# Kernel tuning notes

Measured on AMD Instinct MI355X. Metric: run time of the kernel, lower is better.

Reference implementation:

```python
import jax, jax.numpy as jnp
import numpy as np
import math

B, S, D, H = 2, 2048, 1024, 16
HD = D // H  # head_dims = 64


def setup_inputs() -> dict:
    key = jax.random.key(0)
    ks = jax.random.split(key, 8)
    sc = 1.0 / math.sqrt(D)
    return {
        "queries": jax.random.normal(ks[0], (B, S, D), jnp.float32),
        "keys":    jax.random.normal(ks[1], (B, S, D), jnp.float32),
        "values":  jax.random.normal(ks[2], (B, S, D), jnp.float32),
        # causal mask: 1 where attending allowed, 0 where blocked (masked_fill on ==0)
        "mask": jnp.tril(jnp.ones((S, S), jnp.int32)),
        "Wq": jax.random.normal(ks[3], (D, D), jnp.float32) * sc,
        "bq": jnp.zeros((D,), jnp.float32),
        "Wk": jax.random.normal(ks[4], (D, D), jnp.float32) * sc,
        "bk": jnp.zeros((D,), jnp.float32),
        "Wv": jax.random.normal(ks[5], (D, D), jnp.float32) * sc,
        "bv": jnp.zeros((D,), jnp.float32),
        "Wo": jax.random.normal(ks[6], (D, D), jnp.float32) * sc,
        "bo": jnp.zeros((D,), jnp.float32),
    }


def _split_heads(x):
    # (B, S, D) -> (B, H, S, HD)
    return x.reshape(B, S, H, HD).transpose(0, 2, 1, 3)


def reference(queries, keys, values, mask, Wq, bq, Wk, bk, Wv, bv, Wo, bo):
    q = queries @ Wq + bq
    k = keys @ Wk + bk
    # NOTE: faithful to source quirk — V is projected from the ALREADY-PROJECTED keys
    # (original: keys = self.W_keys(keys); values = self.W_values(keys))
    v = k @ Wv + bv
    q, k, v = _split_heads(q), _split_heads(k), _split_heads(v)
    # naive full NxN attention, as in the source
    scores = jnp.einsum("bhqd,bhkd->bhqk", q, k) / math.sqrt(HD)
    scores = jnp.where(mask == 0, jnp.float32(-1e9), scores)
    probs = jax.nn.softmax(scores, axis=-1)
    attn = jnp.einsum("bhqk,bhkd->bhqd", probs, v)
    attn = attn.transpose(0, 2, 1, 3).reshape(B, S, D)
    return attn @ Wo + bo
```

## Files before the change

kernel.cpp:

```cpp
#include <hip/hip_runtime.h>

typedef unsigned short u16;
typedef unsigned int u32;
typedef __bf16 bf16x8 __attribute__((ext_vector_type(8)));
typedef float f32x4 __attribute__((ext_vector_type(4)));
typedef float f32x16 __attribute__((ext_vector_type(16)));
typedef unsigned int u32x4v __attribute__((ext_vector_type(4)));

#define MFMA16(a, b, c) __builtin_amdgcn_mfma_f32_16x16x32_bf16(a, b, c, 0, 0, 0)
#define MFMA32(a, b, c) __builtin_amdgcn_mfma_f32_32x32x16_bf16(a, b, c, 0, 0, 0)

__device__ __forceinline__ void gload16(const void* g, void* l) {
  __builtin_amdgcn_global_load_lds((const __attribute__((address_space(1))) void*)g,
                                   (__attribute__((address_space(3))) void*)l, 16, 0, 0);
}

__device__ __forceinline__ u16 f2bf(float f) {
  u32 u = __builtin_bit_cast(u32, f);
  u += 0x7fffu + ((u >> 16) & 1u);
  return (u16)(u >> 16);
}
__device__ __forceinline__ u32 pack2(float a, float b) {
  u32 r;
  asm("v_cvt_pk_bf16_f32 %0, %1, %2" : "=v"(r) : "v"(a), "v"(b));
  return r;
}

__global__ __launch_bounds__(256) void cvt_kernel(const float* __restrict__ q,
                                                  const float* __restrict__ k,
                                                  u16* __restrict__ qb,
                                                  u16* __restrict__ kb) {
  const float* src = blockIdx.y ? k : q;
  u16* dst = blockIdx.y ? kb : qb;
  size_t i = (size_t)blockIdx.x * 256 + threadIdx.x;
  float4 v = ((const float4*)src)[i];
  uint2 o;
  o.x = pack2(v.x, v.y);
  o.y = pack2(v.z, v.w);
  ((uint2*)dst)[i] = o;
}

__global__ __launch_bounds__(256) void wtrans_kernel(const float* W0, const float* W1,
                                                     const float* W2, const float* W3,
                                                     u16* T0, u16* T1, u16* T2, u16* T3) {
  int z = blockIdx.z;
  const float* W = z == 0 ? W0 : z == 1 ? W1 : z == 2 ? W2 : W3;
  u16* T = z == 0 ? T0 : z == 1 ? T1 : z == 2 ? T2 : T3;
  __shared__ float tile[64][65];
  int tr = blockIdx.y * 64, tc = blockIdx.x * 64;
  int tid = threadIdx.x;
  int c4 = (tid & 15) * 4, r0 = tid >> 4;
#pragma unroll
  for (int i = 0; i < 4; i++) {
    int r = r0 + i * 16;
    float4 v = *(const float4*)(W + (size_t)(tr + r) * 1024 + tc + c4);
    tile[r][c4 + 0] = v.x; tile[r][c4 + 1] = v.y;
    tile[r][c4 + 2] = v.z; tile[r][c4 + 3] = v.w;
  }
  __syncthreads();
#pragma unroll
  for (int i = 0; i < 2; i++) {
    int c = tid + i * 256;
    int n = c >> 3, kg = c & 7;
    uint4 o;
    o.x = pack2(tile[kg * 8 + 0][n], tile[kg * 8 + 1][n]);
    o.y = pack2(tile[kg * 8 + 2][n], tile[kg * 8 + 3][n]);
    o.z = pack2(tile[kg * 8 + 4][n], tile[kg * 8 + 5][n]);
    o.w = pack2(tile[kg * 8 + 6][n], tile[kg * 8 + 7][n]);
    *(uint4*)(T + (size_t)(tc + n) * 1024 + tr + kg * 8) = o;
  }
}

template <int MODE>
__global__ __launch_bounds__(256) void gemm_kernel(
    const u16* A0, const u16* B0, const float* bias0, void* C0, float scale0,
    const u16* A1, const u16* B1, const float* bias1, void* C1, float scale1,
    int M, int N, int K) {
  const u16* A = A0; const u16* Bt = B0; const float* bias = bias0; void* Cout = C0;
  float scale = scale0;
  if (blockIdx.z) { A = A1; Bt = B1; bias = bias1; Cout = C1; scale = scale1; }

  __shared__ __attribute__((aligned(16))) char sAB[49152];
  const int tid = threadIdx.x, lane = tid & 63, w = tid >> 6;
  const int l15 = lane & 15, quad = lane >> 4;
  const int wm = (w >> 1) * 64, wn = (w & 1) * 32;
  const int m0 = blockIdx.y * 128, n0 = blockIdx.x * 64;

  const int lrow = lane >> 3, lcg = (lane & 7) ^ lrow;
  const u16* aP[4]; const u16* bP[2];
#pragma unroll
  for (int i = 0; i < 4; i++)
    aP[i] = A + (size_t)(m0 + w * 32 + i * 8 + lrow) * K + lcg * 8;
#pragma unroll
  for (int i = 0; i < 2; i++)
    bP[i] = Bt + (size_t)(n0 + w * 16 + i * 8 + lrow) * K + lcg * 8;

  int aoff[4], boff[2];
#pragma unroll
  for (int t = 0; t < 4; t++) {
    int ra = wm + t * 16 + l15;
    aoff[t] = ra * 128 + ((quad ^ (ra & 7)) * 16);
  }
#pragma unroll
  for (int t = 0; t < 2; t++) {
    int rb = wn + t * 16 + l15;
    boff[t] = 16384 + rb * 128 + ((quad ^ (rb & 7)) * 16);
  }

#pragma unroll
  for (int i = 0; i < 4; i++) { gload16(aP[i], sAB + w * 4096 + i * 1024); aP[i] += 64; }
#pragma unroll
  for (int i = 0; i < 2; i++) { gload16(bP[i], sAB + 16384 + w * 2048 + i * 1024); bP[i] += 64; }

  f32x4 acc[4][2] = {};
  int cur = 0;
  for (int k = 0; k < K; k += 64) {
    __syncthreads();
    if (k + 64 < K) {
      char* dst = sAB + (cur ^ 1) * 24576;
#pragma unroll
      for (int i = 0; i < 4; i++) { gload16(aP[i], dst + w * 4096 + i * 1024); aP[i] += 64; }
#pragma unroll
      for (int i = 0; i < 2; i++) { gload16(bP[i], dst + 16384 + w * 2048 + i * 1024); bP[i] += 64; }
    }
    const char* buf = sAB + cur * 24576;
#pragma unroll
    for (int kt = 0; kt < 2; kt++) {
      bf16x8 af[4], bfr[2];
#pragma unroll
      for (int t = 0; t < 4; t++) af[t] = *(const bf16x8*)(buf + (aoff[t] ^ (kt * 64)));
#pragma unroll
      for (int t = 0; t < 2; t++) bfr[t] = *(const bf16x8*)(buf + (boff[t] ^ (kt * 64)));
#pragma unroll
      for (int mt = 0; mt < 4; mt++)
#pragma unroll
        for (int nt = 0; nt < 2; nt++)
          acc[mt][nt] = MFMA16(af[mt], bfr[nt], acc[mt][nt]);
    }
    cur ^= 1;
  }

#pragma unroll
  for (int nt = 0; nt < 2; nt++) {
    int col = n0 + wn + nt * 16 + l15;
    float bv = bias[col];
#pragma unroll
    for (int mt = 0; mt < 4; mt++) {
      int row = m0 + wm + mt * 16 + quad * 4;
      if (MODE == 0) {
        u16* C = (u16*)Cout;
#pragma unroll
        for (int r = 0; r < 4; r++)
          C[(size_t)(row + r) * N + col] = f2bf((acc[mt][nt][r] + bv) * scale);
      } else if (MODE == 1) {
        u16* C = (u16*)Cout;
        int hh = col >> 6, hd = col & 63;
        int bb = row >> 11, s = row & 2047;
        uint2 o;
        o.x = pack2((acc[mt][nt][0] + bv) * scale, (acc[mt][nt][1] + bv) * scale);
        o.y = pack2((acc[mt][nt][2] + bv) * scale, (acc[mt][nt][3] + bv) * scale);
        *(uint2*)(C + ((size_t)((bb * 16 + hh) * 64 + hd) * 2048 + s)) = o;
      } else {
        float* C = (float*)Cout;
#pragma unroll
        for (int r = 0; r < 4; r++)
          C[(size_t)(row + r) * N + col] = (acc[mt][nt][r] + bv) * scale;
      }
    }
  }
}

__global__ __launch_bounds__(256, 2) void attn_kernel(const u16* __restrict__ qw,
                                                      const u16* __restrict__ kw,
                                                      const u16* __restrict__ vw,
                                                      u16* __restrict__ aout) {
  __shared__ __attribute__((aligned(16))) char sKV[4][16384];
  __shared__ float slq[4][64];
  char* sflat = (char*)sKV;
  const int bh = blockIdx.x, p = blockIdx.y;
  const int b = bh >> 4, h = bh & 15;
  const int tid = threadIdx.x, lane = tid & 63, w = tid >> 6;
  const int g = w & 1, kh = w >> 1;
  const int c = lane & 31, hi = lane >> 5;
  const int lrow = lane >> 3, lcg = (lane & 7) ^ lrow;
  const u16* kb0 = kw + (size_t)(b * 2048) * 1024 + h * 64;
  const u16* vb0 = vw + (size_t)bh * 64 * 2048;

  int koffK[4], koffV[2][2];
  {
    int krow = kh * 32 + c;
#pragma unroll
    for (int kt = 0; kt < 4; kt++)
      koffK[kt] = krow * 128 + (((kt * 2 + hi) ^ (krow & 7)) * 16);
#pragma unroll
    for (int m = 0; m < 2; m++) {
      int vrow = m * 32 + c;
#pragma unroll
      for (int kt2 = 0; kt2 < 2; kt2++)
        koffV[m][kt2] = 8192 + vrow * 128 + ((((kh * 2 + kt2) * 2 + hi) ^ (vrow & 7)) * 16);
    }
  }

  auto stage = [&](int j, int slot) {
    char* dst = sKV[slot];
#pragma unroll
    for (int i = 0; i < 2; i++) {
      int rr = w * 16 + i * 8 + lrow;
      gload16(kb0 + (size_t)(j * 64 + rr) * 1024 + lcg * 8, dst + w * 2048 + i * 1024);
      gload16(vb0 + (size_t)rr * 2048 + j * 64 + lcg * 8, dst + 8192 + w * 2048 + i * 1024);
    }
  };

  for (int phase = 0; phase < 2; ++phase) {
    const int t = phase ? (31 - p) : p;
    __syncthreads();

    bf16x8 qf[2][4];
#pragma unroll
    for (int qb2 = 0; qb2 < 2; qb2++) {
      const u16* qbase =
          qw + (size_t)(b * 2048 + t * 64 + qb2 * 32 + c) * 1024 + h * 64 + hi * 8;
#pragma unroll
      for (int kt = 0; kt < 4; kt++) qf[qb2][kt] = *(const bf16x8*)(qbase + kt * 16);
    }
    stage(0, 0);
    if (t >= 1) stage(1, 1);

    f32x16 o00 = {}, o01 = {}, o10 = {}, o11 = {};
    float ls0 = 0.f, ls1 = 0.f;
    const int R = (t + 2) >> 1;
    for (int r = 0; r < R; ++r) {
      __syncthreads();
      if (2 * r + 2 <= t) stage(2 * r + 2, (2 * r + 2) & 3);
      if (2 * r + 3 <= t) stage(2 * r + 3, (2 * r + 3) & 3);
      const int jg = 2 * r + g;
      if (jg <= t) {
        const char* buf = sKV[jg & 3];
        f32x16 S0 = {}, S1 = {};
        __builtin_amdgcn_s_setprio(1);
#pragma unroll
        for (int kt = 0; kt < 4; kt++) {
          bf16x8 kf = *(const bf16x8*)(buf + koffK[kt]);
          S0 = MFMA32(kf, qf[0][kt], S0);
          S1 = MFMA32(kf, qf[1][kt], S1);
        }
        __builtin_amdgcn_s_setprio(0);
        const bool diag = (jg == t);
        u32 pw0[8], pw1[8];
        auto epack = [&](const f32x16& S, int qc, u32* pw, float& ls) {
          float e[16];
#pragma unroll
          for (int rg = 0; rg < 16; rg++) {
            float ev = __builtin_amdgcn_exp2f(S[rg]);
            if (diag) {
              int row = kh * 32 + (rg & 3) + 8 * (rg >> 2) + 4 * hi;
              if (row > qc) ev = 0.f;
            }
            e[rg] = ev;
          }
          float s = 0.f;
#pragma unroll
          for (int rg = 0; rg < 16; rg += 4)
            s += (e[rg] + e[rg + 1]) + (e[rg + 2] + e[rg + 3]);
          ls += s;
#pragma unroll
          for (int i = 0; i < 8; i++) pw[i] = pack2(e[2 * i], e[2 * i + 1]);
        };
        epack(S0, c, pw0, ls0);
        epack(S1, 32 + c, pw1, ls1);
        __builtin_amdgcn_s_setprio(1);
#pragma unroll
        for (int kt2 = 0; kt2 < 2; kt2++) {
          const int bb = kt2 * 4;
          auto a0 = __builtin_amdgcn_permlane32_swap(pw0[bb + 0], pw0[bb + 2], false, false);
          auto a1 = __builtin_amdgcn_permlane32_swap(pw0[bb + 1], pw0[bb + 3], false, false);
          u32x4v pq0 = {a0[0], a1[0], a0[1], a1[1]};
          bf16x8 pf0 = __builtin_bit_cast(bf16x8, pq0);
          auto b0 = __builtin_amdgcn_permlane32_swap(pw1[bb + 0], pw1[bb + 2], false, false);
          auto b1 = __builtin_amdgcn_permlane32_swap(pw1[bb + 1], pw1[bb + 3], false, false);
          u32x4v pq1 = {b0[0], b1[0], b0[1], b1[1]};
          bf16x8 pf1 = __builtin_bit_cast(bf16x8, pq1);
          bf16x8 v0 = *(const bf16x8*)(buf + koffV[0][kt2]);
          bf16x8 v1 = *(const bf16x8*)(buf + koffV[1][kt2]);
          o00 = MFMA32(v0, pf0, o00);
          o10 = MFMA32(v1, pf0, o10);
          o01 = MFMA32(v0, pf1, o01);
          o11 = MFMA32(v1, pf1, o11);
        }
        __builtin_amdgcn_s_setprio(0);
      }
    }

    ls0 += __shfl_xor(ls0, 32, 64);
    ls1 += __shfl_xor(ls1, 32, 64);
    __syncthreads();
    {
      char* myr = sflat + w * 16384;
      auto putq = [&](int qid, const f32x16& v) {
#pragma unroll
        for (int ch = 0; ch < 4; ch++) {
          f32x4 x = {v[ch * 4 + 0], v[ch * 4 + 1], v[ch * 4 + 2], v[ch * 4 + 3]};
          *(f32x4*)(myr + (qid * 4 + ch) * 1024 + lane * 16) = x;
        }
      };
      putq(0, o00); putq(1, o01); putq(2, o10); putq(3, o11);
      slq[w][hi * 32 + c] = hi ? ls1 : ls0;
    }
    __syncthreads();
    {
      f32x16 acc = {};
#pragma unroll
      for (int wv = 0; wv < 4; wv++)
#pragma unroll
        for (int ch = 0; ch < 4; ch++) {
          f32x4 rr = *(const f32x4*)(sflat + wv * 16384 + (w * 4 + ch) * 1024 + lane * 16);
          acc[ch * 4 + 0] += rr[0]; acc[ch * 4 + 1] += rr[1];
          acc[ch * 4 + 2] += rr[2]; acc[ch * 4 + 3] += rr[3];
        }
      const int q = (w & 1) * 32 + c;
      float lt = ((slq[0][q] + slq[1][q]) + (slq[2][q] + slq[3][q]));
      float inv = 1.0f / lt;
      int token = b * 2048 + t * 64 + q;
      u16* outp = aout + (size_t)token * 1024 + h * 64 + (w >> 1) * 32;
#pragma unroll
      for (int i = 0; i < 4; i++) {
        uint2 ov;
        ov.x = pack2(acc[4 * i + 0] * inv, acc[4 * i + 1] * inv);
        ov.y = pack2(acc[4 * i + 2] * inv, acc[4 * i + 3] * inv);
        *(uint2*)(outp + i * 8 + hi * 4) = ov;
      }
    }
  }
}

extern "C" void kernel_launch(void* const* d_in, const int* in_sizes, int n_in,
                              void* d_out, int out_size, void* d_ws, size_t ws_size,
                              hipStream_t stream) {
  const float* queries = (const float*)d_in[0];
  const float* keys    = (const float*)d_in[1];
  const float* Wq = (const float*)d_in[4];
  const float* bq = (const float*)d_in[5];
  const float* Wk = (const float*)d_in[6];
  const float* bk = (const float*)d_in[7];
  const float* Wv = (const float*)d_in[8];
  const float* bv = (const float*)d_in[9];
  const float* Wo = (const float*)d_in[10];
  const float* bo = (const float*)d_in[11];

  char* ws = (char*)d_ws;
  u16* qb  = (u16*)(ws);
  u16* kb  = (u16*)(ws + (8u << 20));
  u16* qP  = (u16*)(ws + (16u << 20));
  u16* kP  = (u16*)(ws);
  u16* vP  = (u16*)(ws + (8u << 20));
  u16* WqT = (u16*)(ws + (24u << 20));
  u16* WkT = (u16*)(ws + (26u << 20));
  u16* WvT = (u16*)(ws + (28u << 20));
  u16* WoT = (u16*)(ws + (30u << 20));

  const float kscale = 1.4426950408889634f / 8.0f;

  cvt_kernel<<<dim3(4096, 2), 256, 0, stream>>>(queries, keys, qb, kb);
  wtrans_kernel<<<dim3(16, 16, 4), 256, 0, stream>>>(Wq, Wk, Wv, Wo, WqT, WkT, WvT, WoT);
  gemm_kernel<0><<<dim3(16, 32, 2), 256, 0, stream>>>(
      qb, WqT, bq, qP, kscale, kb, WkT, bk, kP, 1.0f, 4096, 1024, 1024);
  gemm_kernel<1><<<dim3(16, 32, 1), 256, 0, stream>>>(
      kP, WvT, bv, vP, 1.0f, kP, WvT, bv, vP, 1.0f, 4096, 1024, 1024);
  attn_kernel<<<dim3(32, 16), 256, 0, stream>>>(qP, kP, vP, qP);
  gemm_kernel<2><<<dim3(16, 32, 1), 256, 0, stream>>>(
      qP, WoT, bo, d_out, 1.0f, qP, WoT, bo, d_out, 1.0f, 4096, 1024, 1024);
}
```

Before: 215.4 us.

## Split attention waves by query half, double-buffer KV tiles, raise occupancy

Changes the attention work split. Before, each wave took alternating KV tiles for all 64 queries, with a 4-slot buffer. Now each wave owns a 32-query half and a 32-key half of every tile, and a 2-slot double buffer is used. Shared memory drops from 64KB to 32KB, the cross-wave reduction becomes a single pairwise add, and launch bounds rise to 3 blocks per CU for more occupancy. In exchange there is one barrier per KV tile instead of per pair, so there is less lookahead in prefetching.

New measurement: 221.8 us. +3.0%, slower.

```diff
diff --git a/kernel.cpp b/kernel.cpp
--- a/kernel.cpp
+++ b/kernel.cpp
@@ -170,17 +170,17 @@
   }
 }
 
-__global__ __launch_bounds__(256, 2) void attn_kernel(const u16* __restrict__ qw,
+__global__ __launch_bounds__(256, 3) void attn_kernel(const u16* __restrict__ qw,
                                                       const u16* __restrict__ kw,
                                                       const u16* __restrict__ vw,
                                                       u16* __restrict__ aout) {
-  __shared__ __attribute__((aligned(16))) char sKV[4][16384];
-  __shared__ float slq[4][64];
-  char* sflat = (char*)sKV;
+  __shared__ __attribute__((aligned(16))) char sK[2][16384];
+  __shared__ float slq[2][64];
+  char* sflat = (char*)sK;
   const int bh = blockIdx.x, p = blockIdx.y;
   const int b = bh >> 4, h = bh & 15;
   const int tid = threadIdx.x, lane = tid & 63, w = tid >> 6;
-  const int g = w & 1, kh = w >> 1;
+  const int qh = w & 1, kh = w >> 1;
   const int c = lane & 31, hi = lane >> 5;
   const int lrow = lane >> 3, lcg = (lane & 7) ^ lrow;
   const u16* kb0 = kw + (size_t)(b * 2048) * 1024 + h * 64;
@@ -202,7 +202,7 @@
   }
 
   auto stage = [&](int j, int slot) {
-    char* dst = sKV[slot];
+    char* dst = sK[slot];
 #pragma unroll
     for (int i = 0; i < 2; i++) {
       int rr = w * 16 + i * 8 + lrow;
@@ -215,119 +215,104 @@
     const int t = phase ? (31 - p) : p;
     __syncthreads();
 
-    bf16x8 qf[2][4];
-#pragma unroll
-    for (int qb2 = 0; qb2 < 2; qb2++) {
+    bf16x8 qf[4];
+    {
       const u16* qbase =
-          qw + (size_t)(b * 2048 + t * 64 + qb2 * 32 + c) * 1024 + h * 64 + hi * 8;
-#pragma unroll
-      for (int kt = 0; kt < 4; kt++) qf[qb2][kt] = *(const bf16x8*)(qbase + kt * 16);
+          qw + (size_t)(b * 2048 + t * 64 + qh * 32 + c) * 1024 + h * 64 + hi * 8;
+#pragma unroll
+      for (int kt = 0; kt < 4; kt++) qf[kt] = *(const bf16x8*)(qbase + kt * 16);
     }
     stage(0, 0);
-    if (t >= 1) stage(1, 1);
-
-    f32x16 o00 = {}, o01 = {}, o10 = {}, o11 = {};
-    float ls0 = 0.f, ls1 = 0.f;
-    const int R = (t + 2) >> 1;
-    for (int r = 0; r < R; ++r) {
+
+    f32x16 o0 = {}, o1 = {};
+    float ls = 0.f;
+    for (int j = 0; j <= t; ++j) {
       __syncthreads();
-      if (2 * r + 2 <= t) stage(2 * r + 2, (2 * r + 2) & 3);
-      if (2 * r + 3 <= t) stage(2 * r + 3, (2 * r + 3) & 3);
-      const int jg = 2 * r + g;
-      if (jg <= t) {
-        const char* buf = sKV[jg & 3];
-        f32x16 S0 = {}, S1 = {};
-        __builtin_amdgcn_s_setprio(1);
-#pragma unroll
-        for (int kt = 0; kt < 4; kt++) {
-          bf16x8 kf = *(const bf16x8*)(buf + koffK[kt]);
-          S0 = MFMA32(kf, qf[0][kt], S0);
-          S1 = MFMA32(kf, qf[1][kt], S1);
+      if (j < t) stage(j + 1, (j + 1) & 1);
+      const char* buf = sK[j & 1];
+      f32x16 S = {};
+      __builtin_amdgcn_s_setprio(1);
+#pragma unroll
+      for (int kt = 0; kt < 4; kt++) {
+        bf16x8 kf = *(const bf16x8*)(buf + koffK[kt]);
+        S = MFMA32(kf, qf[kt], S);
+      }
+      __builtin_amdgcn_s_setprio(0);
+      const bool diag = (j == t);
+      u32 pw[8];
+      {
+        float e[16];
+#pragma unroll
+        for (int rg = 0; rg < 16; rg++) {
+          float ev = __builtin_amdgcn_exp2f(S[rg]);
+          if (diag) {
+            int row = kh * 32 + (rg & 3) + 8 * (rg >> 2) + 4 * hi;
+            if (row > qh * 32 + c) ev = 0.f;
+          }
+          e[rg] = ev;
         }
-        __builtin_amdgcn_s_setprio(0);
-        const bool diag = (jg == t);
-        u32 pw0[8], pw1[8];
-        auto epack = [&](const f32x16& S, int qc, u32* pw, float& ls) {
-          float e[16];
-#pragma unroll
-          for (int rg = 0; rg < 16; rg++) {
-            float ev = __builtin_amdgcn_exp2f(S[rg]);
-            if (diag) {
-              int row = kh * 32 + (rg & 3) + 8 * (rg >> 2) + 4 * hi;
-              if (row > qc) ev = 0.f;
-            }
-            e[rg] = ev;
-          }
-          float s = 0.f;
-#pragma unroll
-          for (int rg = 0; rg < 16; rg += 4)
-            s += (e[rg] + e[rg + 1]) + (e[rg + 2] + e[rg + 3]);
-          ls += s;
-#pragma unroll
-          for (int i = 0; i < 8; i++) pw[i] = pack2(e[2 * i], e[2 * i + 1]);
-        };
-        epack(S0, c, pw0, ls0);
-        epack(S1, 32 + c, pw1, ls1);
-        __builtin_amdgcn_s_setprio(1);
-#pragma unroll
-        for (int kt2 = 0; kt2 < 2; kt2++) {
-          const int bb = kt2 * 4;
-          auto a0 = __builtin_amdgcn_permlane32_swap(pw0[bb + 0], pw0[bb + 2], false, false);
-          auto a1 = __builtin_amdgcn_permlane32_swap(pw0[bb + 1], pw0[bb + 3], false, false);
-          u32x4v pq0 = {a0[0], a1[0], a0[1], a1[1]};
-          bf16x8 pf0 = __builtin_bit_cast(bf16x8, pq0);
-          auto b0 = __builtin_amdgcn_permlane32_swap(pw1[bb + 0], pw1[bb + 2], false, false);
-          auto b1 = __builtin_amdgcn_permlane32_swap(pw1[bb + 1], pw1[bb + 3], false, false);
-          u32x4v pq1 = {b0[0], b1[0], b0[1], b1[1]};
-          bf16x8 pf1 = __builtin_bit_cast(bf16x8, pq1);
-          bf16x8 v0 = *(const bf16x8*)(buf + koffV[0][kt2]);
-          bf16x8 v1 = *(const bf16x8*)(buf + koffV[1][kt2]);
-          o00 = MFMA32(v0, pf0, o00);
-          o10 = MFMA32(v1, pf0, o10);
-          o01 = MFMA32(v0, pf1, o01);
-          o11 = MFMA32(v1, pf1, o11);
-        }
-        __builtin_amdgcn_s_setprio(0);
-      }
-    }
-
-    ls0 += __shfl_xor(ls0, 32, 64);
-    ls1 += __shfl_xor(ls1, 32, 64);
+        float sAcc = 0.f;
+#pragma unroll
+        for (int rg = 0; rg < 16; rg += 4)
+          sAcc += (e[rg] + e[rg + 1]) + (e[rg + 2] + e[rg + 3]);
+        ls += sAcc;
+#pragma unroll
+        for (int i = 0; i < 8; i++) pw[i] = pack2(e[2 * i], e[2 * i + 1]);
+      }
+      __builtin_amdgcn_s_setprio(1);
+#pragma unroll
+      for (int kt2 = 0; kt2 < 2; kt2++) {
+        const int bb = kt2 * 4;
+        auto a0 = __builtin_amdgcn_permlane32_swap(pw[bb + 0], pw[bb + 2], false, false);
+        auto a1 = __builtin_amdgcn_permlane32_swap(pw[bb + 1], pw[bb + 3], false, false);
+        u32x4v pq = {a0[0], a1[0], a0[1], a1[1]};
+        bf16x8 pf = __builtin_bit_cast(bf16x8, pq);
+        bf16x8 v0 = *(const bf16x8*)(buf + koffV[0][kt2]);
+        bf16x8 v1 = *(const bf16x8*)(buf + koffV[1][kt2]);
+        o0 = MFMA32(v0, pf, o0);
+        o1 = MFMA32(v1, pf, o1);
+      }
+      __builtin_amdgcn_s_setprio(0);
+    }
+
+    ls += __shfl_xor(ls, 32, 64);
     __syncthreads();
-    {
-      char* myr = sflat + w * 16384;
-      auto putq = [&](int qid, const f32x16& v) {
-#pragma unroll
-        for (int ch = 0; ch < 4; ch++) {
-          f32x4 x = {v[ch * 4 + 0], v[ch * 4 + 1], v[ch * 4 + 2], v[ch * 4 + 3]};
-          *(f32x4*)(myr + (qid * 4 + ch) * 1024 + lane * 16) = x;
-        }
-      };
-      putq(0, o00); putq(1, o01); putq(2, o10); putq(3, o11);
-      slq[w][hi * 32 + c] = hi ? ls1 : ls0;
+    if (kh == 1) {
+      char* myr = sflat + qh * 8192;
+#pragma unroll
+      for (int ch = 0; ch < 4; ch++) {
+        f32x4 x0 = {o0[ch * 4 + 0], o0[ch * 4 + 1], o0[ch * 4 + 2], o0[ch * 4 + 3]};
+        *(f32x4*)(myr + ch * 1024 + lane * 16) = x0;
+        f32x4 x1 = {o1[ch * 4 + 0], o1[ch * 4 + 1], o1[ch * 4 + 2], o1[ch * 4 + 3]};
+        *(f32x4*)(myr + 4096 + ch * 1024 + lane * 16) = x1;
+      }
+      slq[qh][c] = ls;
     }
     __syncthreads();
-    {
-      f32x16 acc = {};
-#pragma unroll
-      for (int wv = 0; wv < 4; wv++)
-#pragma unroll
-        for (int ch = 0; ch < 4; ch++) {
-          f32x4 rr = *(const f32x4*)(sflat + wv * 16384 + (w * 4 + ch) * 1024 + lane * 16);
-          acc[ch * 4 + 0] += rr[0]; acc[ch * 4 + 1] += rr[1];
-          acc[ch * 4 + 2] += rr[2]; acc[ch * 4 + 3] += rr[3];
-        }
-      const int q = (w & 1) * 32 + c;
-      float lt = ((slq[0][q] + slq[1][q]) + (slq[2][q] + slq[3][q]));
+    if (kh == 0) {
+      const char* pr = sflat + qh * 8192;
+#pragma unroll
+      for (int ch = 0; ch < 4; ch++) {
+        f32x4 r0 = *(const f32x4*)(pr + ch * 1024 + lane * 16);
+        o0[ch * 4 + 0] += r0[0]; o0[ch * 4 + 1] += r0[1];
+        o0[ch * 4 + 2] += r0[2]; o0[ch * 4 + 3] += r0[3];
+        f32x4 r1 = *(const f32x4*)(pr + 4096 + ch * 1024 + lane * 16);
+        o1[ch * 4 + 0] += r1[0]; o1[ch * 4 + 1] += r1[1];
+        o1[ch * 4 + 2] += r1[2]; o1[ch * 4 + 3] += r1[3];
+      }
+      float lt = ls + slq[qh][c];
       float inv = 1.0f / lt;
-      int token = b * 2048 + t * 64 + q;
-      u16* outp = aout + (size_t)token * 1024 + h * 64 + (w >> 1) * 32;
-#pragma unroll
-      for (int i = 0; i < 4; i++) {
+      int token = b * 2048 + t * 64 + qh * 32 + c;
+      u16* outp = aout + (size_t)token * 1024 + h * 64;
+#pragma unroll
+      for (int ch = 0; ch < 4; ch++) {
         uint2 ov;
-        ov.x = pack2(acc[4 * i + 0] * inv, acc[4 * i + 1] * inv);
-        ov.y = pack2(acc[4 * i + 2] * inv, acc[4 * i + 3] * inv);
-        *(uint2*)(outp + i * 8 + hi * 4) = ov;
+        ov.x = pack2(o0[ch * 4 + 0] * inv, o0[ch * 4 + 1] * inv);
+        ov.y = pack2(o0[ch * 4 + 2] * inv, o0[ch * 4 + 3] * inv);
+        *(uint2*)(outp + ch * 8 + hi * 4) = ov;
+        ov.x = pack2(o1[ch * 4 + 0] * inv, o1[ch * 4 + 1] * inv);
+        ov.y = pack2(o1[ch * 4 + 2] * inv, o1[ch * 4 + 3] * inv);
+        *(uint2*)(outp + 32 + ch * 8 + hi * 4) = ov;
       }
     }
   }
```
